# Kernel tuning notes

Measured on AMD Instinct MI355X. Metric: run time of the kernel, lower is better.

The kernel has to match this reference:

```python
import jax, jax.numpy as jnp
import numpy as np

N, E = 50000, 800000
IN, HID, OUT, H = 128, 16, 16, 4


def setup_inputs() -> dict:
    key = jax.random.key(0)
    ks = jax.random.split(key, 11)
    sc = 0.1
    return {
        "features": jax.random.normal(ks[0], (N, IN), jnp.float32),
        "src": jax.random.randint(ks[1], (E,), 0, N, dtype=jnp.int64) if jax.config.jax_enable_x64 else jax.random.randint(ks[1], (E,), 0, N).astype(jnp.int32),
        "dst": jax.random.randint(ks[2], (E,), 0, N).astype(jnp.int32),
        "W1": jax.random.normal(ks[3], (H * HID, IN), jnp.float32) * sc,
        "al1": jax.random.normal(ks[4], (H, HID), jnp.float32) * sc,
        "ar1": jax.random.normal(ks[5], (H, HID), jnp.float32) * sc,
        "b1": jax.random.normal(ks[6], (H * HID,), jnp.float32) * sc,
        "W2": jax.random.normal(ks[7], (H * OUT, H * HID), jnp.float32) * sc,
        "al2": jax.random.normal(ks[8], (H, OUT), jnp.float32) * sc,
        "ar2": jax.random.normal(ks[9], (H, OUT), jnp.float32) * sc,
        "b2": jax.random.normal(ks[10], (H * OUT,), jnp.float32) * sc,
    }


def gat_conv(src, dst, feat, W, al, ar, b, heads, dout):
    """DGL-style GATConv: fc -> edge attention -> dst-softmax -> scatter-sum."""
    n = feat.shape[0]
    h = (feat @ W.T).reshape(n, heads, dout)            # [N,H,D]
    el = jnp.einsum("nhd,hd->nh", h, al)                # [N,H]
    er = jnp.einsum("nhd,hd->nh", h, ar)                # [N,H]
    e = jax.nn.leaky_relu(el[src] + er[dst], 0.2)       # [E,H]
    m = jax.ops.segment_max(e, dst, num_segments=n)     # per-dst max, [N,H]
    a = jnp.exp(e - m[dst])                             # [E,H]
    s = jax.ops.segment_sum(a, dst, num_segments=n)     # [N,H]
    alpha = a / s[dst]                                  # edge softmax, [E,H]
    out = jax.ops.segment_sum(alpha[:, :, None] * h[src], dst, num_segments=n)
    return out + b.reshape(1, heads, dout)              # [N,H,D]


def reference(features, src, dst, W1, al1, ar1, b1, W2, al2, ar2, b2):
    h = gat_conv(src, dst, features, W1, al1, ar1, b1, H, HID).reshape(N, H * HID)
    h = jax.nn.relu(h)
    h = gat_conv(src, dst, h, W2, al2, ar2, b2, H, OUT).mean(axis=1)  # mean over heads
    return jax.nn.log_softmax(h, axis=1)
```

## Files before the change

### kernel.cpp

```cpp
#include <hip/hip_runtime.h>
#include <math.h>

#define N_NODES 50000
#define N_EDGES 800000
#define NPART 8
#define PART_SZ ((N_NODES + NPART - 1) / NPART)
#define CAP 64
#define SCAT_BLOCKS 2048

typedef __attribute__((ext_vector_type(8))) short short8;
typedef __attribute__((ext_vector_type(8))) unsigned short ushort8;
typedef __attribute__((ext_vector_type(4))) float v4f;
typedef __attribute__((ext_vector_type(4))) int int4v;

__device__ __forceinline__ float bf2f(unsigned short h) {
    return __uint_as_float(((unsigned int)h) << 16);
}
__device__ __forceinline__ unsigned short f2bf(float f) {
    unsigned int u = __float_as_uint(f);
    u += 0x7fff + ((u >> 16) & 1);
    return (unsigned short)(u >> 16);
}

__device__ __forceinline__ short8 load_afrag(const float* X, size_t row, int K,
                                             int kc, int quad) {
    const float* p = X + row * K + kc * 32 + quad * 8;
    const float4 t0 = *(const float4*)p;
    const float4 t1 = *(const float4*)(p + 4);
    short8 a;
    a[0] = (short)f2bf(t0.x); a[1] = (short)f2bf(t0.y);
    a[2] = (short)f2bf(t0.z); a[3] = (short)f2bf(t0.w);
    a[4] = (short)f2bf(t1.x); a[5] = (short)f2bf(t1.y);
    a[6] = (short)f2bf(t1.z); a[7] = (short)f2bf(t1.w);
    return a;
}
__device__ __forceinline__ short8 load_afrag(const unsigned short* X, size_t row,
                                             int K, int kc, int quad) {
    return *(const short8*)(X + row * K + kc * 32 + quad * 8);
}

template <int K, typename XT>
__global__ __launch_bounds__(256) void fc_att_mfma(
    const XT* __restrict__ X, const float* __restrict__ W,
    const float* __restrict__ al, const float* __restrict__ ar,
    unsigned short* __restrict__ Hout, float* __restrict__ el,
    float* __restrict__ er, int nTiles)
{
    constexpr int KP = K + 4;
    constexpr int NKC = K / 32;
    __shared__ float Wlds[64 * KP];
    const int tid = threadIdx.x;
    for (int i = tid; i < 64 * K; i += 256) {
        int r = i / K, c = i - r * K;
        Wlds[r * KP + c] = W[i];
    }
    __syncthreads();

    const int lane = tid & 63;
    const int wave = tid >> 6;
    const int d = lane & 15;
    const int quad = lane >> 4;

    short8 wf[4][NKC];
#pragma unroll
    for (int ng = 0; ng < 4; ++ng) {
#pragma unroll
        for (int kc = 0; kc < NKC; ++kc) {
            const float* wp = &Wlds[(ng * 16 + d) * KP + kc * 32 + quad * 8];
            const v4f w0 = *(const v4f*)wp;
            const v4f w1 = *(const v4f*)(wp + 4);
            short8 f;
            f[0] = (short)f2bf(w0[0]); f[1] = (short)f2bf(w0[1]);
            f[2] = (short)f2bf(w0[2]); f[3] = (short)f2bf(w0[3]);
            f[4] = (short)f2bf(w1[0]); f[5] = (short)f2bf(w1[1]);
            f[6] = (short)f2bf(w1[2]); f[7] = (short)f2bf(w1[3]);
            wf[ng][kc] = f;
        }
    }

    const int tile = blockIdx.x * 4 + wave;
    if (tile >= nTiles) return;
    const int node0 = tile * 16;

    v4f cc[4] = {{0.f,0.f,0.f,0.f},{0.f,0.f,0.f,0.f},{0.f,0.f,0.f,0.f},{0.f,0.f,0.f,0.f}};
#pragma unroll
    for (int kc = 0; kc < NKC; ++kc) {
        const short8 a = load_afrag(X, (size_t)(node0 + d), K, kc, quad);
        cc[0] = __builtin_amdgcn_mfma_f32_16x16x32_bf16(a, wf[0][kc], cc[0], 0, 0, 0);
        cc[1] = __builtin_amdgcn_mfma_f32_16x16x32_bf16(a, wf[1][kc], cc[1], 0, 0, 0);
        cc[2] = __builtin_amdgcn_mfma_f32_16x16x32_bf16(a, wf[2][kc], cc[2], 0, 0, 0);
        cc[3] = __builtin_amdgcn_mfma_f32_16x16x32_bf16(a, wf[3][kc], cc[3], 0, 0, 0);
    }

#pragma unroll
    for (int ng = 0; ng < 4; ++ng) {
        const float alv = al[ng * 16 + d];
        const float arv = ar[ng * 16 + d];
        const v4f c = cc[ng];
#pragma unroll
        for (int r = 0; r < 4; ++r) {
            const int node = node0 + quad * 4 + r;
            Hout[(size_t)node * 64 + ng * 16 + d] = f2bf(c[r]);
            float vel = c[r] * alv;
            float ver = c[r] * arv;
#pragma unroll
            for (int off = 1; off < 16; off <<= 1) {
                vel += __shfl_xor(vel, off);
                ver += __shfl_xor(ver, off);
            }
            if (d == 0) {
                el[node * 4 + ng] = vel;
                er[node * 4 + ng] = ver;
            }
        }
    }
}

__device__ __forceinline__ void scat1(int d, int s, int lo, int hi,
                                      int* __restrict__ cnt16,
                                      unsigned short* __restrict__ col)
{
    if (d >= lo && d < hi) {
        const int pos = atomicAdd(&cnt16[(unsigned)d * 16], 1);
        if (pos < CAP) col[(unsigned)d * CAP + pos] = (unsigned short)s;
    }
}

__global__ __launch_bounds__(256) void scatter_bucket_kernel(
    const int* __restrict__ src, const int* __restrict__ dst,
    int* __restrict__ cnt16, unsigned short* __restrict__ col)
{
    const int part = blockIdx.x & (NPART - 1);
    const int lo = part * PART_SZ;
    const int hi = lo + PART_SZ;
    const int tid_p = ((int)blockIdx.x >> 3) * 256 + threadIdx.x;
    const int stride = (SCAT_BLOCKS / NPART) * 256;
    const int4v* dst4 = (const int4v*)dst;
    const int4v* src4 = (const int4v*)src;
    const int NQ = N_EDGES / 4;
    for (int q = tid_p; q < NQ; q += 2 * stride) {
        const int q2 = q + stride;
        const bool ok2 = q2 < NQ;
        const int4v dA = __builtin_nontemporal_load(dst4 + q);
        const int4v sA = __builtin_nontemporal_load(src4 + q);
        const int4v dB = ok2 ? __builtin_nontemporal_load(dst4 + q2) : (int4v){-1,-1,-1,-1};
        const int4v sB = ok2 ? __builtin_nontemporal_load(src4 + q2) : (int4v){0,0,0,0};
        scat1(dA[0], sA[0], lo, hi, cnt16, col);
        scat1(dA[1], sA[1], lo, hi, cnt16, col);
        scat1(dA[2], sA[2], lo, hi, cnt16, col);
        scat1(dA[3], sA[3], lo, hi, cnt16, col);
        scat1(dB[0], sB[0], lo, hi, cnt16, col);
        scat1(dB[1], sB[1], lo, hi, cnt16, col);
        scat1(dB[2], sB[2], lo, hi, cnt16, col);
        scat1(dB[3], sB[3], lo, hi, cnt16, col);
    }
}

__device__ __forceinline__ void agg_walk(
    const unsigned short* __restrict__ colrow, int len,
    const float* __restrict__ el, const unsigned short* __restrict__ Hf,
    int head, int lane, float erv_a, float& acc_out, float& sacc_out)
{
    const int j_a = lane >> 2;
    const unsigned h_a = (unsigned)(lane & 3);
    const unsigned ul = (unsigned)lane;
    float acc0 = 0.f, acc1 = 0.f, acc2 = 0.f, acc3 = 0.f;
    float sacc_a = 0.f;
    for (int i = 0; i < len; i += 16) {
        const ushort8 sv0 = __builtin_nontemporal_load((const ushort8*)(colrow + i));
        const ushort8 sv1 = __builtin_nontemporal_load((const ushort8*)(colrow + i + 8));
        const int rm = len - i;
        const unsigned s_a = (unsigned)colrow[i + j_a];
        float x = el[s_a * 4u + h_a] + erv_a;
        x = fmaxf(x, 0.2f * x);
        float a = __expf(x);
        a = (j_a < rm) ? a : 0.f;
        sacc_a += a;
        float hh[16];
#pragma unroll
        for (int j = 0; j < 8; ++j) hh[j] = bf2f(Hf[(unsigned)sv0[j] * 64u + ul]);
#pragma unroll
        for (int j = 0; j < 8; ++j) hh[8 + j] = bf2f(Hf[(unsigned)sv1[j] * 64u + ul]);
#pragma unroll
        for (int j = 0; j < 16; ++j) {
            const float aj = __shfl(a, j * 4 + head);
            if ((j & 3) == 0) acc0 = fmaf(aj, hh[j], acc0);
            else if ((j & 3) == 1) acc1 = fmaf(aj, hh[j], acc1);
            else if ((j & 3) == 2) acc2 = fmaf(aj, hh[j], acc2);
            else acc3 = fmaf(aj, hh[j], acc3);
        }
    }
    sacc_a += __shfl_xor(sacc_a, 4);
    sacc_a += __shfl_xor(sacc_a, 8);
    sacc_a += __shfl_xor(sacc_a, 16);
    sacc_a += __shfl_xor(sacc_a, 32);
    sacc_out = __shfl(sacc_a, head);
    acc_out = (acc0 + acc1) + (acc2 + acc3);
}

__global__ __launch_bounds__(256) void agg_relu_kernel(
    const int* __restrict__ cnt16, const unsigned short* __restrict__ col,
    const float* __restrict__ el, const float* __restrict__ er,
    const unsigned short* __restrict__ Hf, const float* __restrict__ b,
    unsigned short* __restrict__ out, int n)
{
    const int lane = threadIdx.x & 63;
    const int head = lane >> 4;
    const int node = blockIdx.x * 4 + (threadIdx.x >> 6);
    if (node >= n) return;
    const float erv_a = er[node * 4 + (lane & 3)];
    const int len = min(cnt16[(unsigned)node * 16], CAP);
    float acc, sacc;
    agg_walk(col + (unsigned)node * CAP, len, el, Hf, head, lane, erv_a, acc, sacc);
    float v = sacc > 0.f ? acc / sacc : 0.f;
    v += b[lane];
    __builtin_nontemporal_store(f2bf(v > 0.f ? v : 0.f), out + (size_t)node * 64 + lane);
}

__global__ __launch_bounds__(256) void agg_final_kernel(
    const int* __restrict__ cnt16, const unsigned short* __restrict__ col,
    const float* __restrict__ el, const float* __restrict__ er,
    const unsigned short* __restrict__ Hf, const float* __restrict__ b,
    float* __restrict__ out, int n)
{
    const int lane = threadIdx.x & 63;
    const int head = lane >> 4;
    const int node = blockIdx.x * 4 + (threadIdx.x >> 6);
    if (node >= n) return;
    const float erv_a = er[node * 4 + (lane & 3)];
    const int len = min(cnt16[(unsigned)node * 16], CAP);
    float acc, sacc;
    agg_walk(col + (unsigned)node * CAP, len, el, Hf, head, lane, erv_a, acc, sacc);
    float z = sacc > 0.f ? acc / sacc : 0.f;
    z += b[lane];
    z += __shfl_xor(z, 16);
    z += __shfl_xor(z, 32);
    z *= 0.25f;
    float m = z;
#pragma unroll
    for (int off = 1; off < 16; off <<= 1) m = fmaxf(m, __shfl_xor(m, off));
    float ex = __expf(z - m);
    float se = ex;
#pragma unroll
    for (int off = 1; off < 16; off <<= 1) se += __shfl_xor(se, off);
    if (lane < 16)
        __builtin_nontemporal_store(z - m - __logf(se), out + (size_t)node * 16 + lane);
}

extern "C" void kernel_launch(void* const* d_in, const int* in_sizes, int n_in,
                              void* d_out, int out_size, void* d_ws, size_t ws_size,
                              hipStream_t stream)
{
    const float* feat = (const float*)d_in[0];
    const int*   src  = (const int*)d_in[1];
    const int*   dst  = (const int*)d_in[2];
    const float* W1   = (const float*)d_in[3];
    const float* al1  = (const float*)d_in[4];
    const float* ar1  = (const float*)d_in[5];
    const float* b1   = (const float*)d_in[6];
    const float* W2   = (const float*)d_in[7];
    const float* al2  = (const float*)d_in[8];
    const float* ar2  = (const float*)d_in[9];
    const float* b2   = (const float*)d_in[10];
    float* out = (float*)d_out;

    float* el  = (float*)d_ws;
    float* er  = el + N_NODES * 4;
    int*   cnt16 = (int*)(er + N_NODES * 4);
    uintptr_t p = ((uintptr_t)(cnt16 + N_NODES * 16) + 15) & ~(uintptr_t)15;
    unsigned short* col = (unsigned short*)p;
    unsigned short* A   = col + (size_t)N_NODES * CAP + 64;
    unsigned short* B   = A + (size_t)N_NODES * 64;

    const int NT = N_NODES / 16;
    const int FB = (NT + 3) / 4;
    const int AB = (N_NODES + 3) / 4;

    hipMemsetAsync(cnt16, 0, (size_t)N_NODES * 16 * sizeof(int), stream);
    scatter_bucket_kernel<<<SCAT_BLOCKS, 256, 0, stream>>>(src, dst, cnt16, col);

    fc_att_mfma<128, float><<<FB, 256, 0, stream>>>(feat, W1, al1, ar1, A, el, er, NT);
    agg_relu_kernel<<<AB, 256, 0, stream>>>(cnt16, col, el, er, A, b1, B, N_NODES);

    fc_att_mfma<64, unsigned short><<<FB, 256, 0, stream>>>(B, W2, al2, ar2, A, el, er, NT);
    agg_final_kernel<<<AB, 256, 0, stream>>>(cnt16, col, el, er, A, b2, out, N_NODES);
}
```

Measured before the change: 217.9 us.

## Process two nodes per wavefront with packed bf16x2 gathers in aggregation

The aggregation kernels now map two destination nodes onto one 64-lane wavefront, 32 lanes each. Each lane gathers one 32-bit word holding two bf16 features and keeps low and high accumulators, so the walk advances 8 edges per step instead of 16. The aim is fewer gather instructions and better lane utilisation for short neighbour lists. In exchange, both half-waves loop to the longer of the two lengths, and the col buffer is now zeroed by the memset so padded slots are safe to read, which adds memset traffic.

```diff
diff --git a/kernel.cpp b/kernel.cpp
--- a/kernel.cpp
+++ b/kernel.cpp
@@ -11,6 +11,7 @@
 typedef __attribute__((ext_vector_type(8))) short short8;
 typedef __attribute__((ext_vector_type(8))) unsigned short ushort8;
 typedef __attribute__((ext_vector_type(4))) float v4f;
+typedef __attribute__((ext_vector_type(2))) float v2f;
 typedef __attribute__((ext_vector_type(4))) int int4v;
 
 __device__ __forceinline__ float bf2f(unsigned short h) {
@@ -156,19 +157,19 @@
     }
 }
 
-__device__ __forceinline__ void agg_walk(
-    const unsigned short* __restrict__ colrow, int len,
-    const float* __restrict__ el, const unsigned short* __restrict__ Hf,
-    int head, int lane, float erv_a, float& acc_out, float& sacc_out)
-{
-    const int j_a = lane >> 2;
-    const unsigned h_a = (unsigned)(lane & 3);
-    const unsigned ul = (unsigned)lane;
-    float acc0 = 0.f, acc1 = 0.f, acc2 = 0.f, acc3 = 0.f;
+__device__ __forceinline__ void agg_walk_pair(
+    const unsigned short* __restrict__ colrow, int len, int len_max,
+    const float* __restrict__ el, const unsigned int* __restrict__ Hf32,
+    int hb, int hl, float erv_a,
+    float& accL_out, float& accH_out, float& sacc_a_out)
+{
+    const int j_a = hl >> 2;
+    const unsigned h_a = (unsigned)(hl & 3);
+    const int hd = hl >> 3;
+    float accL0 = 0.f, accL1 = 0.f, accH0 = 0.f, accH1 = 0.f;
     float sacc_a = 0.f;
-    for (int i = 0; i < len; i += 16) {
-        const ushort8 sv0 = __builtin_nontemporal_load((const ushort8*)(colrow + i));
-        const ushort8 sv1 = __builtin_nontemporal_load((const ushort8*)(colrow + i + 8));
+    for (int i = 0; i < len_max; i += 8) {
+        const ushort8 sv = __builtin_nontemporal_load((const ushort8*)(colrow + i));
         const int rm = len - i;
         const unsigned s_a = (unsigned)colrow[i + j_a];
         float x = el[s_a * 4u + h_a] + erv_a;
@@ -176,75 +177,98 @@
         float a = __expf(x);
         a = (j_a < rm) ? a : 0.f;
         sacc_a += a;
-        float hh[16];
-#pragma unroll
-        for (int j = 0; j < 8; ++j) hh[j] = bf2f(Hf[(unsigned)sv0[j] * 64u + ul]);
-#pragma unroll
-        for (int j = 0; j < 8; ++j) hh[8 + j] = bf2f(Hf[(unsigned)sv1[j] * 64u + ul]);
-#pragma unroll
-        for (int j = 0; j < 16; ++j) {
-            const float aj = __shfl(a, j * 4 + head);
-            if ((j & 3) == 0) acc0 = fmaf(aj, hh[j], acc0);
-            else if ((j & 3) == 1) acc1 = fmaf(aj, hh[j], acc1);
-            else if ((j & 3) == 2) acc2 = fmaf(aj, hh[j], acc2);
-            else acc3 = fmaf(aj, hh[j], acc3);
+        unsigned uu[8];
+#pragma unroll
+        for (int j = 0; j < 8; ++j)
+            uu[j] = Hf32[(unsigned)sv[j] * 32u + (unsigned)hl];
+#pragma unroll
+        for (int j = 0; j < 8; ++j) {
+            const float aj = __shfl(a, hb + j * 4 + hd);
+            const float lo = __uint_as_float(uu[j] << 16);
+            const float hi = __uint_as_float(uu[j] & 0xffff0000u);
+            if (j & 1) { accL1 = fmaf(aj, lo, accL1); accH1 = fmaf(aj, hi, accH1); }
+            else       { accL0 = fmaf(aj, lo, accL0); accH0 = fmaf(aj, hi, accH0); }
         }
     }
     sacc_a += __shfl_xor(sacc_a, 4);
     sacc_a += __shfl_xor(sacc_a, 8);
     sacc_a += __shfl_xor(sacc_a, 16);
-    sacc_a += __shfl_xor(sacc_a, 32);
-    sacc_out = __shfl(sacc_a, head);
-    acc_out = (acc0 + acc1) + (acc2 + acc3);
+    sacc_a_out = sacc_a;
+    accL_out = accL0 + accL1;
+    accH_out = accH0 + accH1;
 }
 
 __global__ __launch_bounds__(256) void agg_relu_kernel(
     const int* __restrict__ cnt16, const unsigned short* __restrict__ col,
     const float* __restrict__ el, const float* __restrict__ er,
-    const unsigned short* __restrict__ Hf, const float* __restrict__ b,
-    unsigned short* __restrict__ out, int n)
+    const unsigned int* __restrict__ Hf32, const float* __restrict__ b,
+    unsigned int* __restrict__ out32, int n)
 {
     const int lane = threadIdx.x & 63;
-    const int head = lane >> 4;
-    const int node = blockIdx.x * 4 + (threadIdx.x >> 6);
+    const int wave = threadIdx.x >> 6;
+    const int hl = lane & 31;
+    const int hb = lane & 32;
+    const int node = blockIdx.x * 8 + wave * 2 + (lane >> 5);
     if (node >= n) return;
-    const float erv_a = er[node * 4 + (lane & 3)];
+    const int hd = hl >> 3;
+    const int cg = hd * 16 + (hl & 7) * 2;
+    const float erv_a = er[node * 4 + (hl & 3)];
     const int len = min(cnt16[(unsigned)node * 16], CAP);
-    float acc, sacc;
-    agg_walk(col + (unsigned)node * CAP, len, el, Hf, head, lane, erv_a, acc, sacc);
-    float v = sacc > 0.f ? acc / sacc : 0.f;
-    v += b[lane];
-    __builtin_nontemporal_store(f2bf(v > 0.f ? v : 0.f), out + (size_t)node * 64 + lane);
+    const int len_max = max(len, __shfl_xor(len, 32));
+    float accL, accH, sacc_a;
+    agg_walk_pair(col + (unsigned)node * CAP, len, len_max, el, Hf32,
+                  hb, hl, erv_a, accL, accH, sacc_a);
+    const float sc = __shfl(sacc_a, hb + hd);
+    float vL = sc > 0.f ? accL / sc : 0.f;
+    float vH = sc > 0.f ? accH / sc : 0.f;
+    vL += b[cg];   vH += b[cg + 1];
+    vL = vL > 0.f ? vL : 0.f;
+    vH = vH > 0.f ? vH : 0.f;
+    const unsigned u = (unsigned)f2bf(vL) | ((unsigned)f2bf(vH) << 16);
+    __builtin_nontemporal_store(u, out32 + (size_t)node * 32 + hl);
 }
 
 __global__ __launch_bounds__(256) void agg_final_kernel(
     const int* __restrict__ cnt16, const unsigned short* __restrict__ col,
     const float* __restrict__ el, const float* __restrict__ er,
-    const unsigned short* __restrict__ Hf, const float* __restrict__ b,
+    const unsigned int* __restrict__ Hf32, const float* __restrict__ b,
     float* __restrict__ out, int n)
 {
     const int lane = threadIdx.x & 63;
-    const int head = lane >> 4;
-    const int node = blockIdx.x * 4 + (threadIdx.x >> 6);
+    const int wave = threadIdx.x >> 6;
+    const int hl = lane & 31;
+    const int hb = lane & 32;
+    const int node = blockIdx.x * 8 + wave * 2 + (lane >> 5);
     if (node >= n) return;
-    const float erv_a = er[node * 4 + (lane & 3)];
+    const int hd = hl >> 3;
+    const int cg = hd * 16 + (hl & 7) * 2;
+    const float erv_a = er[node * 4 + (hl & 3)];
     const int len = min(cnt16[(unsigned)node * 16], CAP);
-    float acc, sacc;
-    agg_walk(col + (unsigned)node * CAP, len, el, Hf, head, lane, erv_a, acc, sacc);
-    float z = sacc > 0.f ? acc / sacc : 0.f;
-    z += b[lane];
-    z += __shfl_xor(z, 16);
-    z += __shfl_xor(z, 32);
-    z *= 0.25f;
-    float m = z;
-#pragma unroll
-    for (int off = 1; off < 16; off <<= 1) m = fmaxf(m, __shfl_xor(m, off));
-    float ex = __expf(z - m);
-    float se = ex;
-#pragma unroll
-    for (int off = 1; off < 16; off <<= 1) se += __shfl_xor(se, off);
-    if (lane < 16)
-        __builtin_nontemporal_store(z - m - __logf(se), out + (size_t)node * 16 + lane);
+    const int len_max = max(len, __shfl_xor(len, 32));
+    float accL, accH, sacc_a;
+    agg_walk_pair(col + (unsigned)node * CAP, len, len_max, el, Hf32,
+                  hb, hl, erv_a, accL, accH, sacc_a);
+    const float sc = __shfl(sacc_a, hb + hd);
+    float zL = sc > 0.f ? accL / sc : 0.f;
+    float zH = sc > 0.f ? accH / sc : 0.f;
+    zL += b[cg];   zH += b[cg + 1];
+    zL += __shfl_xor(zL, 8);  zL += __shfl_xor(zL, 16);  zL *= 0.25f;
+    zH += __shfl_xor(zH, 8);  zH += __shfl_xor(zH, 16);  zH *= 0.25f;
+    float m = fmaxf(zL, zH);
+    m = fmaxf(m, __shfl_xor(m, 1));
+    m = fmaxf(m, __shfl_xor(m, 2));
+    m = fmaxf(m, __shfl_xor(m, 4));
+    float se = __expf(zL - m) + __expf(zH - m);
+    se += __shfl_xor(se, 1);
+    se += __shfl_xor(se, 2);
+    se += __shfl_xor(se, 4);
+    const float lse = __logf(se);
+    if (hl < 8) {
+        v2f r;
+        r[0] = zL - m - lse;
+        r[1] = zH - m - lse;
+        __builtin_nontemporal_store(r, (v2f*)(out + (size_t)node * 16 + hl * 2));
+    }
 }
 
 extern "C" void kernel_launch(void* const* d_in, const int* in_sizes, int n_in,
@@ -274,14 +298,17 @@
 
     const int NT = N_NODES / 16;
     const int FB = (NT + 3) / 4;
-    const int AB = (N_NODES + 3) / 4;
-
-    hipMemsetAsync(cnt16, 0, (size_t)N_NODES * 16 * sizeof(int), stream);
+    const int AB2 = (N_NODES + 7) / 8;
+
+    (void)hipMemsetAsync(cnt16, 0, (size_t)((char*)A - (char*)cnt16), stream);
     scatter_bucket_kernel<<<SCAT_BLOCKS, 256, 0, stream>>>(src, dst, cnt16, col);
 
     fc_att_mfma<128, float><<<FB, 256, 0, stream>>>(feat, W1, al1, ar1, A, el, er, NT);
-    agg_relu_kernel<<<AB, 256, 0, stream>>>(cnt16, col, el, er, A, b1, B, N_NODES);
+    agg_relu_kernel<<<AB2, 256, 0, stream>>>(cnt16, col, el, er,
+                                             (const unsigned int*)A, b1,
+                                             (unsigned int*)B, N_NODES);
 
     fc_att_mfma<64, unsigned short><<<FB, 256, 0, stream>>>(B, W2, al2, ar2, A, el, er, NT);
-    agg_final_kernel<<<AB, 256, 0, stream>>>(cnt16, col, el, er, A, b2, out, N_NODES);
-}
+    agg_final_kernel<<<AB2, 256, 0, stream>>>(cnt16, col, el, er,
+                                              (const unsigned int*)A, b2, out, N_NODES);
+}
```

Result: faster. 199.0 us (-8.7%).

## Process four nodes per wavefront with 8-byte vectorized feature gathers

Applied to the files above, without the earlier changes.

The aggregation kernels change from one node per 64-lane wavefront to one node per 16-lane quarter-wave. Each lane now gathers four bf16 features as a single 8-byte load and keeps four accumulators, and edges are walked in chunks of 8 instead of 16. This is meant to cut padding waste for low-degree nodes and raise memory-level parallelism per gather. In exchange, divergence grows because the loop runs to the maximum degree among the four nodes. The memset is also widened to zero the column buckets, so padded entries index node 0.

```diff
diff --git a/kernel.cpp b/kernel.cpp
--- a/kernel.cpp
+++ b/kernel.cpp
@@ -11,6 +11,7 @@
 typedef __attribute__((ext_vector_type(8))) short short8;
 typedef __attribute__((ext_vector_type(8))) unsigned short ushort8;
 typedef __attribute__((ext_vector_type(4))) float v4f;
+typedef __attribute__((ext_vector_type(2))) unsigned int u32x2;
 typedef __attribute__((ext_vector_type(4))) int int4v;
 
 __device__ __forceinline__ float bf2f(unsigned short h) {
@@ -156,95 +157,126 @@
     }
 }
 
-__device__ __forceinline__ void agg_walk(
-    const unsigned short* __restrict__ colrow, int len,
-    const float* __restrict__ el, const unsigned short* __restrict__ Hf,
-    int head, int lane, float erv_a, float& acc_out, float& sacc_out)
-{
-    const int j_a = lane >> 2;
-    const unsigned h_a = (unsigned)(lane & 3);
-    const unsigned ul = (unsigned)lane;
-    float acc0 = 0.f, acc1 = 0.f, acc2 = 0.f, acc3 = 0.f;
-    float sacc_a = 0.f;
-    for (int i = 0; i < len; i += 16) {
-        const ushort8 sv0 = __builtin_nontemporal_load((const ushort8*)(colrow + i));
-        const ushort8 sv1 = __builtin_nontemporal_load((const ushort8*)(colrow + i + 8));
+__device__ __forceinline__ void agg_walk_quad(
+    const unsigned short* __restrict__ colrow, int len, int len_max,
+    const float* __restrict__ el, const u32x2* __restrict__ Hf2,
+    int qb, int ql, float erv_a, v4f& acc_out, float& sacc_out)
+{
+    const int j_a = ql >> 2;
+    const unsigned h_a = (unsigned)(ql & 3);
+    const int hq = ql >> 2;
+    v4f acc = {0.f, 0.f, 0.f, 0.f};
+    float sacc = 0.f;
+    for (int i = 0; i < len_max; i += 8) {
+        const ushort8 sv = __builtin_nontemporal_load((const ushort8*)(colrow + i));
         const int rm = len - i;
-        const unsigned s_a = (unsigned)colrow[i + j_a];
-        float x = el[s_a * 4u + h_a] + erv_a;
-        x = fmaxf(x, 0.2f * x);
-        float a = __expf(x);
-        a = (j_a < rm) ? a : 0.f;
-        sacc_a += a;
-        float hh[16];
-#pragma unroll
-        for (int j = 0; j < 8; ++j) hh[j] = bf2f(Hf[(unsigned)sv0[j] * 64u + ul]);
-#pragma unroll
-        for (int j = 0; j < 8; ++j) hh[8 + j] = bf2f(Hf[(unsigned)sv1[j] * 64u + ul]);
-#pragma unroll
-        for (int j = 0; j < 16; ++j) {
-            const float aj = __shfl(a, j * 4 + head);
-            if ((j & 3) == 0) acc0 = fmaf(aj, hh[j], acc0);
-            else if ((j & 3) == 1) acc1 = fmaf(aj, hh[j], acc1);
-            else if ((j & 3) == 2) acc2 = fmaf(aj, hh[j], acc2);
-            else acc3 = fmaf(aj, hh[j], acc3);
+        const unsigned s0 = (unsigned)sv[j_a];
+        const unsigned s1 = (unsigned)sv[4 + j_a];
+        float x0 = el[s0 * 4u + h_a] + erv_a;
+        float x1 = el[s1 * 4u + h_a] + erv_a;
+        x0 = fmaxf(x0, 0.2f * x0);
+        x1 = fmaxf(x1, 0.2f * x1);
+        float a0 = __expf(x0);
+        float a1 = __expf(x1);
+        a0 = (j_a < rm) ? a0 : 0.f;
+        a1 = (j_a + 4 < rm) ? a1 : 0.f;
+        sacc += a0 + a1;
+        u32x2 uu[8];
+#pragma unroll
+        for (int j = 0; j < 8; ++j)
+            uu[j] = Hf2[(unsigned)sv[j] * 16u + (unsigned)ql];
+#pragma unroll
+        for (int j = 0; j < 8; ++j) {
+            const float aj = __shfl(j < 4 ? a0 : a1, qb + ((j & 3) << 2) + hq);
+            acc[0] = fmaf(aj, __uint_as_float(uu[j][0] << 16), acc[0]);
+            acc[1] = fmaf(aj, __uint_as_float(uu[j][0] & 0xffff0000u), acc[1]);
+            acc[2] = fmaf(aj, __uint_as_float(uu[j][1] << 16), acc[2]);
+            acc[3] = fmaf(aj, __uint_as_float(uu[j][1] & 0xffff0000u), acc[3]);
         }
     }
-    sacc_a += __shfl_xor(sacc_a, 4);
-    sacc_a += __shfl_xor(sacc_a, 8);
-    sacc_a += __shfl_xor(sacc_a, 16);
-    sacc_a += __shfl_xor(sacc_a, 32);
-    sacc_out = __shfl(sacc_a, head);
-    acc_out = (acc0 + acc1) + (acc2 + acc3);
+    sacc += __shfl_xor(sacc, 4);
+    sacc += __shfl_xor(sacc, 8);
+    sacc_out = sacc;
+    acc_out = acc;
 }
 
 __global__ __launch_bounds__(256) void agg_relu_kernel(
     const int* __restrict__ cnt16, const unsigned short* __restrict__ col,
     const float* __restrict__ el, const float* __restrict__ er,
-    const unsigned short* __restrict__ Hf, const float* __restrict__ b,
-    unsigned short* __restrict__ out, int n)
+    const u32x2* __restrict__ Hf2, const float* __restrict__ b,
+    u32x2* __restrict__ out2, int n)
 {
     const int lane = threadIdx.x & 63;
-    const int head = lane >> 4;
-    const int node = blockIdx.x * 4 + (threadIdx.x >> 6);
+    const int wave = threadIdx.x >> 6;
+    const int ql = lane & 15;
+    const int qb = lane & 48;
+    const int node = (blockIdx.x * 4 + wave) * 4 + (lane >> 4);
     if (node >= n) return;
-    const float erv_a = er[node * 4 + (lane & 3)];
-    const int len = min(cnt16[(unsigned)node * 16], CAP);
-    float acc, sacc;
-    agg_walk(col + (unsigned)node * CAP, len, el, Hf, head, lane, erv_a, acc, sacc);
-    float v = sacc > 0.f ? acc / sacc : 0.f;
-    v += b[lane];
-    __builtin_nontemporal_store(f2bf(v > 0.f ? v : 0.f), out + (size_t)node * 64 + lane);
+    const int hq = ql >> 2;
+    const int cg = hq * 16 + (ql & 3) * 4;
+    const float erv_a = er[node * 4 + (ql & 3)];
+    int len = min(cnt16[(unsigned)node * 16], CAP);
+    int lm = max(len, __shfl_xor(len, 16));
+    lm = max(lm, __shfl_xor(lm, 32));
+    v4f acc; float sacc;
+    agg_walk_quad(col + (unsigned)node * CAP, len, lm, el, Hf2, qb, ql, erv_a, acc, sacc);
+    const float sc = __shfl(sacc, qb + hq);
+    u32x2 u;
+    float v0 = (sc > 0.f ? acc[0] / sc : 0.f) + b[cg];
+    float v1 = (sc > 0.f ? acc[1] / sc : 0.f) + b[cg + 1];
+    float v2 = (sc > 0.f ? acc[2] / sc : 0.f) + b[cg + 2];
+    float v3 = (sc > 0.f ? acc[3] / sc : 0.f) + b[cg + 3];
+    v0 = fmaxf(v0, 0.f); v1 = fmaxf(v1, 0.f);
+    v2 = fmaxf(v2, 0.f); v3 = fmaxf(v3, 0.f);
+    u[0] = (unsigned)f2bf(v0) | ((unsigned)f2bf(v1) << 16);
+    u[1] = (unsigned)f2bf(v2) | ((unsigned)f2bf(v3) << 16);
+    __builtin_nontemporal_store(u, out2 + (size_t)node * 16 + ql);
 }
 
 __global__ __launch_bounds__(256) void agg_final_kernel(
     const int* __restrict__ cnt16, const unsigned short* __restrict__ col,
     const float* __restrict__ el, const float* __restrict__ er,
-    const unsigned short* __restrict__ Hf, const float* __restrict__ b,
+    const u32x2* __restrict__ Hf2, const float* __restrict__ b,
     float* __restrict__ out, int n)
 {
     const int lane = threadIdx.x & 63;
-    const int head = lane >> 4;
-    const int node = blockIdx.x * 4 + (threadIdx.x >> 6);
+    const int wave = threadIdx.x >> 6;
+    const int ql = lane & 15;
+    const int qb = lane & 48;
+    const int node = (blockIdx.x * 4 + wave) * 4 + (lane >> 4);
     if (node >= n) return;
-    const float erv_a = er[node * 4 + (lane & 3)];
-    const int len = min(cnt16[(unsigned)node * 16], CAP);
-    float acc, sacc;
-    agg_walk(col + (unsigned)node * CAP, len, el, Hf, head, lane, erv_a, acc, sacc);
-    float z = sacc > 0.f ? acc / sacc : 0.f;
-    z += b[lane];
-    z += __shfl_xor(z, 16);
-    z += __shfl_xor(z, 32);
-    z *= 0.25f;
-    float m = z;
-#pragma unroll
-    for (int off = 1; off < 16; off <<= 1) m = fmaxf(m, __shfl_xor(m, off));
-    float ex = __expf(z - m);
-    float se = ex;
-#pragma unroll
-    for (int off = 1; off < 16; off <<= 1) se += __shfl_xor(se, off);
-    if (lane < 16)
-        __builtin_nontemporal_store(z - m - __logf(se), out + (size_t)node * 16 + lane);
+    const int hq = ql >> 2;
+    const int cg = hq * 16 + (ql & 3) * 4;
+    const float erv_a = er[node * 4 + (ql & 3)];
+    int len = min(cnt16[(unsigned)node * 16], CAP);
+    int lm = max(len, __shfl_xor(len, 16));
+    lm = max(lm, __shfl_xor(lm, 32));
+    v4f acc; float sacc;
+    agg_walk_quad(col + (unsigned)node * CAP, len, lm, el, Hf2, qb, ql, erv_a, acc, sacc);
+    const float sc = __shfl(sacc, qb + hq);
+    float z[4];
+#pragma unroll
+    for (int t = 0; t < 4; ++t)
+        z[t] = (sc > 0.f ? acc[t] / sc : 0.f) + b[cg + t];
+#pragma unroll
+    for (int t = 0; t < 4; ++t) {
+        z[t] += __shfl_xor(z[t], 4);
+        z[t] += __shfl_xor(z[t], 8);
+        z[t] *= 0.25f;
+    }
+    float m = fmaxf(fmaxf(z[0], z[1]), fmaxf(z[2], z[3]));
+    m = fmaxf(m, __shfl_xor(m, 1));
+    m = fmaxf(m, __shfl_xor(m, 2));
+    float se = __expf(z[0] - m) + __expf(z[1] - m) + __expf(z[2] - m) + __expf(z[3] - m);
+    se += __shfl_xor(se, 1);
+    se += __shfl_xor(se, 2);
+    const float lse = __logf(se);
+    if (ql < 4) {
+        v4f r;
+#pragma unroll
+        for (int t = 0; t < 4; ++t) r[t] = z[t] - m - lse;
+        __builtin_nontemporal_store(r, (v4f*)(out + (size_t)node * 16 + ql * 4));
+    }
 }
 
 extern "C" void kernel_launch(void* const* d_in, const int* in_sizes, int n_in,
@@ -274,14 +306,17 @@
 
     const int NT = N_NODES / 16;
     const int FB = (NT + 3) / 4;
-    const int AB = (N_NODES + 3) / 4;
-
-    hipMemsetAsync(cnt16, 0, (size_t)N_NODES * 16 * sizeof(int), stream);
+    const int QB = N_NODES / 16;
+
+    (void)hipMemsetAsync(cnt16, 0, (size_t)((char*)A - (char*)cnt16), stream);
     scatter_bucket_kernel<<<SCAT_BLOCKS, 256, 0, stream>>>(src, dst, cnt16, col);
 
     fc_att_mfma<128, float><<<FB, 256, 0, stream>>>(feat, W1, al1, ar1, A, el, er, NT);
-    agg_relu_kernel<<<AB, 256, 0, stream>>>(cnt16, col, el, er, A, b1, B, N_NODES);
+    agg_relu_kernel<<<QB, 256, 0, stream>>>(cnt16, col, el, er,
+                                            (const u32x2*)A, b1,
+                                            (u32x2*)B, N_NODES);
 
     fc_att_mfma<64, unsigned short><<<FB, 256, 0, stream>>>(B, W2, al2, ar2, A, el, er, NT);
-    agg_final_kernel<<<AB, 256, 0, stream>>>(cnt16, col, el, er, A, b2, out, N_NODES);
-}
+    agg_final_kernel<<<QB, 256, 0, stream>>>(cnt16, col, el, er,
+                                             (const u32x2*)A, b2, out, N_NODES);
+}
```

After: 204.1 us. 1.07x faster.
